# Performance work log

Hardware: AMD Instinct MI355X
Metric: run time of the kernel (lower is better)

Reference implementation:

```python
import jax, jax.numpy as jnp
import numpy as np

N_NODES = 40000
N_EDGES = 640000
IN_CH = 128
HID_CH = 128
OUT_CH = 121


def setup_inputs() -> dict:
    key = jax.random.key(0)
    ks = jax.random.split(key, 6)
    x = jax.random.normal(ks[0], (N_NODES, IN_CH), dtype=jnp.float32)
    edge_index = jax.random.randint(ks[1], (2, N_EDGES), 0, N_NODES, dtype=jnp.int64)

    def xavier(k, shape):
        fan_out, fan_in = shape
        lim = np.sqrt(6.0 / (fan_in + fan_out)).astype(np.float32)
        return jax.random.uniform(k, shape, jnp.float32, -lim, lim)

    W1l = xavier(ks[2], (HID_CH, IN_CH))
    W1r = xavier(ks[3], (HID_CH, IN_CH))
    W2l = xavier(ks[4], (OUT_CH, HID_CH))
    W2r = xavier(ks[5], (OUT_CH, HID_CH))
    b1l = jnp.zeros((HID_CH,), jnp.float32)
    b1r = jnp.zeros((HID_CH,), jnp.float32)
    b2l = jnp.zeros((OUT_CH,), jnp.float32)
    b2r = jnp.zeros((OUT_CH,), jnp.float32)
    return {"x": x, "edge_index": edge_index,
            "W1l": W1l, "b1l": b1l, "W1r": W1r, "b1r": b1r,
            "W2l": W2l, "b2l": b2l, "W2r": W2r, "b2r": b2r}


def _sage_conv(h, src, dst, Wl, bl, Wr, br):
    # mean aggregation of source-node features onto destinations
    msg = h[src]                                             # [E, C]
    agg = jax.ops.segment_sum(msg, dst, num_segments=N_NODES)
    cnt = jax.ops.segment_sum(jnp.ones((src.shape[0],), h.dtype), dst,
                              num_segments=N_NODES)
    agg = agg / jnp.maximum(cnt, 1.0)[:, None]
    # out = lin_l(agg) + lin_r(h)
    return agg @ Wl.T + bl + h @ Wr.T + br


def reference(x, edge_index, W1l, b1l, W1r, b1r, W2l, b2l, W2r, b2r):
    src, dst = edge_index[0], edge_index[1]
    h = jax.nn.relu(_sage_conv(x, src, dst, W1l, b1l, W1r, b1r))
    # dropout is identity in inference mode
    return _sage_conv(h, src, dst, W2l, b2l, W2r, b2r)
```

## Files before the change

kernel.cpp:

```cpp
#include <hip/hip_runtime.h>


#define NCH 128
#define CAPX 16
#define EPT 8

typedef __bf16 bf16x8 __attribute__((ext_vector_type(8)));
typedef float f32x4 __attribute__((ext_vector_type(4)));
typedef unsigned short ushort8 __attribute__((ext_vector_type(8)));

static __device__ __forceinline__ unsigned short f2b(float f) {
  return __builtin_bit_cast(unsigned short, static_cast<__bf16>(f));
}
static __device__ __forceinline__ float b2f(unsigned short u) {
  union { unsigned int i; float f; } v;
  v.i = ((unsigned int)u) << 16;
  return v.f;
}

__global__ __launch_bounds__(256) void k_main(
    const int* __restrict__ src, const int* __restrict__ dst, int E,
    int* __restrict__ cntx, unsigned short* __restrict__ slotu,
    int* __restrict__ ovf_n, int2* __restrict__ ovf,
    const float* __restrict__ x, unsigned short* __restrict__ xb, int n4,
    const float* __restrict__ W1l, const float* __restrict__ W1r,
    const float* __restrict__ b1l, const float* __restrict__ b1r,
    const float* __restrict__ W2l, const float* __restrict__ W2r,
    const float* __restrict__ b2l, const float* __restrict__ b2r,
    unsigned short* __restrict__ pack1, unsigned short* __restrict__ pack2,
    float* __restrict__ bsum1, float* __restrict__ bsum2, int NOUT,
    int nbBkt, int nbCvt) {
  int blk = blockIdx.x;
  if (blk < nbBkt) {
    unsigned int xcc;
    asm volatile("s_getreg_b32 %0, hwreg(HW_REG_XCC_ID)" : "=s"(xcc));
    xcc &= 7u;
    const int base = blk * (256 * EPT) + (int)threadIdx.x;
    int d[EPT], s[EPT], pos[EPT];
#pragma unroll
    for (int j = 0; j < EPT; ++j) {
      const int e = base + j * 256;
      const bool ok = e < E;
      d[j] = ok ? dst[e] : -1;
      s[j] = ok ? src[e] : 0;
    }
#pragma unroll
    for (int j = 0; j < EPT; ++j) {
      pos[j] = (d[j] >= 0)
          ? __hip_atomic_fetch_add(&cntx[(long)d[j] * 8 + xcc], 1,
                                   __ATOMIC_RELAXED, __HIP_MEMORY_SCOPE_WORKGROUP)
          : 0;
    }
#pragma unroll
    for (int j = 0; j < EPT; ++j) {
      if (d[j] >= 0) {
        if (pos[j] < CAPX)
          slotu[(long)d[j] * 128 + xcc * CAPX + pos[j]] = (unsigned short)s[j];
        else {
          int o = atomicAdd(ovf_n, 1);
          ovf[o] = make_int2(d[j], s[j]);
        }
      }
    }
    return;
  }
  blk -= nbBkt;
  if (blk < nbCvt) {
    int i = blk * 256 + threadIdx.x;
    if (i < n4) {
      float4 v = ((const float4*)x)[i];
      ushort4 r;
      r.x = f2b(v.x); r.y = f2b(v.y); r.z = f2b(v.z); r.w = f2b(v.w);
      ((ushort4*)xb)[i] = r;
    }
    return;
  }
  blk -= nbCvt;
  const int layer = blk >> 4;
  const float* Wl = layer ? W2l : W1l;
  const float* Wr = layer ? W2r : W1r;
  const float* bl = layer ? b2l : b1l;
  const float* br = layer ? b2r : b1r;
  unsigned short* pack = layer ? pack2 : pack1;
  float* bsum = layer ? bsum2 : bsum1;
  const int NO = layer ? NOUT : NCH;
  int tid = (blk & 15) * 256 + threadIdx.x;
  int c = tid >> 9;
  int t = (tid >> 6) & 7;
  int l = tid & 63;
  int n = t * 16 + (l & 15);
  int kb = c * 32 + ((l >> 4) << 3);
  unsigned short o[8];
#pragma unroll
  for (int j = 0; j < 8; ++j) {
    int k = kb + j;
    float v = 0.f;
    if (n < NO) v = (k < 128) ? Wl[n * 128 + k] : Wr[n * 128 + (k - 128)];
    o[j] = f2b(v);
  }
  ushort4 lo, hi;
  lo.x = o[0]; lo.y = o[1]; lo.z = o[2]; lo.w = o[3];
  hi.x = o[4]; hi.y = o[5]; hi.z = o[6]; hi.w = o[7];
  *(ushort4*)(pack + (long)tid * 8) = lo;
  *(ushort4*)(pack + (long)tid * 8 + 4) = hi;
  if (tid < 128) bsum[tid] = (tid < NO) ? (bl[tid] + br[tid]) : 0.f;
}

__global__ __launch_bounds__(256) void k_agg(
    const unsigned short* __restrict__ feat, const int* __restrict__ cntx,
    const unsigned short* __restrict__ slotu, const int* __restrict__ ovf_n,
    const int2* __restrict__ ovf, unsigned short* __restrict__ agg, int N) {
  __shared__ unsigned short list[16][128];
  __shared__ int degs[16], ms[16];
  const int lg = threadIdx.x >> 4;
  const int ln = threadIdx.x & 15;
  const int g = blockIdx.x * 16 + lg;

  if (g < N) {
    const int4 cA = *(const int4*)(cntx + (long)g * 8);
    const int4 cB = *(const int4*)(cntx + (long)g * 8 + 4);
    const int c[8] = {cA.x, cA.y, cA.z, cA.w, cB.x, cB.y, cB.z, cB.w};
    int deg = 0, p = 0, myoff = 0, mycc = 0;
#pragma unroll
    for (int xx = 0; xx < 8; ++xx) {
      const int cc = (c[xx] < CAPX) ? c[xx] : CAPX;
      if (ln == xx) { myoff = p; mycc = cc; }
      p += cc;
      deg += c[xx];
    }
    if (ln == 0) { degs[lg] = deg; ms[lg] = p; }
    if (ln < 8 && mycc > 0) {
      const unsigned short* sp = slotu + (long)g * 128 + ln * CAPX;
      for (int i = 0; i < mycc; ++i) list[lg][myoff + i] = sp[i];
    }
  } else if (ln == 0) {
    degs[lg] = 0; ms[lg] = 0;
  }
  __syncthreads();

  if (g >= N) return;
  const int m = ms[lg];
  const int col = ln * 8;
  const unsigned short* fcol = feat + col;

  float acc[8];
#pragma unroll
  for (int k = 0; k < 8; ++k) acc[k] = 0.f;

  const unsigned short* __restrict__ il = list[lg];
  int j = 0;
  for (; j + 7 < m; j += 8) {
    const int i0 = il[j + 0], i1 = il[j + 1], i2 = il[j + 2], i3 = il[j + 3];
    const int i4 = il[j + 4], i5 = il[j + 5], i6 = il[j + 6], i7 = il[j + 7];
    const ushort8 v0 = *(const ushort8*)(fcol + (long)i0 * NCH);
    const ushort8 v1 = *(const ushort8*)(fcol + (long)i1 * NCH);
    const ushort8 v2 = *(const ushort8*)(fcol + (long)i2 * NCH);
    const ushort8 v3 = *(const ushort8*)(fcol + (long)i3 * NCH);
    const ushort8 v4 = *(const ushort8*)(fcol + (long)i4 * NCH);
    const ushort8 v5 = *(const ushort8*)(fcol + (long)i5 * NCH);
    const ushort8 v6 = *(const ushort8*)(fcol + (long)i6 * NCH);
    const ushort8 v7 = *(const ushort8*)(fcol + (long)i7 * NCH);
#pragma unroll
    for (int k = 0; k < 8; ++k) {
      acc[k] += b2f(v0[k]); acc[k] += b2f(v1[k]);
      acc[k] += b2f(v2[k]); acc[k] += b2f(v3[k]);
      acc[k] += b2f(v4[k]); acc[k] += b2f(v5[k]);
      acc[k] += b2f(v6[k]); acc[k] += b2f(v7[k]);
    }
  }
  if (j + 3 < m) {
    const int i0 = il[j + 0], i1 = il[j + 1], i2 = il[j + 2], i3 = il[j + 3];
    const ushort8 v0 = *(const ushort8*)(fcol + (long)i0 * NCH);
    const ushort8 v1 = *(const ushort8*)(fcol + (long)i1 * NCH);
    const ushort8 v2 = *(const ushort8*)(fcol + (long)i2 * NCH);
    const ushort8 v3 = *(const ushort8*)(fcol + (long)i3 * NCH);
#pragma unroll
    for (int k = 0; k < 8; ++k) {
      acc[k] += b2f(v0[k]); acc[k] += b2f(v1[k]);
      acc[k] += b2f(v2[k]); acc[k] += b2f(v3[k]);
    }
    j += 4;
  }
  for (; j < m; ++j) {
    const ushort8 v = *(const ushort8*)(fcol + (long)il[j] * NCH);
#pragma unroll
    for (int k = 0; k < 8; ++k) acc[k] += b2f(v[k]);
  }

  const int on = *ovf_n;
  for (int o = 0; o < on; ++o) {
    const int2 p = ovf[o];
    if (p.x == g) {
      const ushort8 v = *(const ushort8*)(fcol + (long)p.y * NCH);
#pragma unroll
      for (int k = 0; k < 8; ++k) acc[k] += b2f(v[k]);
    }
  }

  const int deg = degs[lg];
  const int dd = (deg < 1) ? 1 : deg;
  const float inv = 1.f / (float)dd;
  ushort8 r;
#pragma unroll
  for (int k = 0; k < 8; ++k) r[k] = f2b(acc[k] * inv);
  *(ushort8*)(agg + (long)g * NCH + col) = r;
}

__global__ __launch_bounds__(256) void k_gemm(
    const unsigned short* __restrict__ Ag,
    const unsigned short* __restrict__ Sf,
    const unsigned short* __restrict__ pack,
    const float* __restrict__ bsum,
    unsigned short* __restrict__ outb,
    float* __restrict__ outf,
    int M, int NO, int do_relu) {
  const int wave = threadIdx.x >> 6;
  const int lane = threadIdx.x & 63;
  const int R = blockIdx.x * 128 + wave * 32;
  const int mrow = lane & 15;
  const int koct = (lane >> 4) * 8;

  int r0 = R + mrow;       if (r0 > M - 1) r0 = M - 1;
  int r1 = R + 16 + mrow;  if (r1 > M - 1) r1 = M - 1;

  f32x4 acc[2][8];
#pragma unroll
  for (int mt = 0; mt < 2; ++mt)
#pragma unroll
    for (int t = 0; t < 8; ++t) acc[mt][t] = (f32x4){0.f, 0.f, 0.f, 0.f};

#pragma unroll
  for (int c = 0; c < 8; ++c) {
    const unsigned short* __restrict__ Abase = (c < 4) ? Ag : Sf;
    const int k0 = (c & 3) * 32;
    const bf16x8 a0 = *(const bf16x8*)(Abase + (long)r0 * NCH + k0 + koct);
    const bf16x8 a1 = *(const bf16x8*)(Abase + (long)r1 * NCH + k0 + koct);
    const unsigned short* bp = pack + ((long)(c * 8) * 64 + lane) * 8;
#pragma unroll
    for (int t = 0; t < 8; ++t) {
      const bf16x8 bfrag = *(const bf16x8*)(bp + (long)t * 512);
      acc[0][t] = __builtin_amdgcn_mfma_f32_16x16x32_bf16(a0, bfrag, acc[0][t], 0, 0, 0);
      acc[1][t] = __builtin_amdgcn_mfma_f32_16x16x32_bf16(a1, bfrag, acc[1][t], 0, 0, 0);
    }
  }

  const int nloc = lane & 15;
  const int rquad = (lane >> 4) * 4;
#pragma unroll
  for (int mt = 0; mt < 2; ++mt) {
#pragma unroll
    for (int t = 0; t < 8; ++t) {
      const int n = t * 16 + nloc;
      const float bias = bsum[n];
#pragma unroll
      for (int r = 0; r < 4; ++r) {
        const int m = R + mt * 16 + rquad + r;
        if (m < M && n < NO) {
          float v = acc[mt][t][r] + bias;
          if (do_relu) v = fmaxf(v, 0.f);
          if (outb) outb[(long)m * NCH + n] = f2b(v);
          else outf[(long)m * NO + n] = v;
        }
      }
    }
  }
}


extern "C" void kernel_launch(void* const* d_in, const int* in_sizes, int n_in,
                              void* d_out, int out_size, void* d_ws, size_t ws_size,
                              hipStream_t stream) {
  const float* x = (const float*)d_in[0];
  const int* ei = (const int*)d_in[1];
  const float* W1l = (const float*)d_in[2];
  const float* b1l = (const float*)d_in[3];
  const float* W1r = (const float*)d_in[4];
  const float* b1r = (const float*)d_in[5];
  const float* W2l = (const float*)d_in[6];
  const float* b2l = (const float*)d_in[7];
  const float* W2r = (const float*)d_in[8];
  const float* b2r = (const float*)d_in[9];
  float* out = (float*)d_out;

  const int N = in_sizes[0] / NCH;
  const int E = in_sizes[1] / 2;
  const int NOUT = out_size / N;

  const int* src = ei;
  const int* dst = ei + E;

  char* w = (char*)d_ws;
  auto alloc = [&](size_t bytes) {
    char* p = w;
    w += (bytes + 255) & ~(size_t)255;
    return p;
  };
  unsigned short* xb = (unsigned short*)alloc((size_t)N * NCH * 2);
  unsigned short* hb = (unsigned short*)alloc((size_t)N * NCH * 2);
  unsigned short* aggb = (unsigned short*)alloc((size_t)N * NCH * 2);
  unsigned short* pack1 = (unsigned short*)alloc(8 * 8 * 64 * 8 * 2);
  unsigned short* pack2 = (unsigned short*)alloc(8 * 8 * 64 * 8 * 2);
  float* bsum1 = (float*)alloc(128 * 4);
  float* bsum2 = (float*)alloc(128 * 4);
  int* cntx = (int*)alloc(((size_t)N * 8 + 1) * 4);
  int* ovf_n = cntx + (size_t)N * 8;
  unsigned short* slotu = (unsigned short*)alloc((size_t)N * 128 * 2);
  int2* ovf = (int2*)alloc((size_t)E * 8);

  const int n4 = N * NCH / 4;
  const int nbBkt = (E + 256 * EPT - 1) / (256 * EPT);
  const int nbCvt = (n4 + 255) / 256;

  hipMemsetAsync(cntx, 0, ((size_t)N * 8 + 1) * 4, stream);

  k_main<<<nbBkt + nbCvt + 32, 256, 0, stream>>>(
      src, dst, E, cntx, slotu, ovf_n, ovf,
      x, xb, n4,
      W1l, W1r, b1l, b1r, W2l, W2r, b2l, b2r,
      pack1, pack2, bsum1, bsum2, NOUT, nbBkt, nbCvt);

  const int gaggr = (N + 15) / 16;
  const int gblk = (N + 127) / 128;

  k_agg<<<gaggr, 256, 0, stream>>>(xb, cntx, slotu, ovf_n, ovf, aggb, N);
  k_gemm<<<gblk, 256, 0, stream>>>(aggb, xb, pack1, bsum1, hb, (float*)nullptr,
                                   N, NCH, 1);
  k_agg<<<gaggr, 256, 0, stream>>>(hb, cntx, slotu, ovf_n, ovf, aggb, N);
  k_gemm<<<gblk, 256, 0, stream>>>(aggb, hb, pack2, bsum2, (unsigned short*)nullptr,
                                   out, N, NOUT, 0);
}
```

Measured before the change: 204.0 us.

## Fuse all stages into one persistent cooperative kernel with grid-wide syncs

Replaces the memset plus five kernel launches with a single cooperative persistent kernel that runs setup, bucketing, two aggregations and two GEMMs as grid-strided phases separated by grid.sync(). The memset of the count array moves into the setup phase. The aim is to remove launch gaps and the memset call. The grid is capped at 1024 blocks, so the gather-heavy aggregation may get less latency hiding than the original 2500-block launch, and each grid barrier adds its own cost. A fallback path launches the phases as separate kernels if the cooperative launch fails.

After: 213.4 us. 4.6% more time.

```diff
diff --git a/kernel.cpp b/kernel.cpp
--- a/kernel.cpp
+++ b/kernel.cpp
@@ -1,4 +1,7 @@
 #include <hip/hip_runtime.h>
+#include <hip/hip_cooperative_groups.h>
+
+namespace cg = cooperative_groups;
 
 
 #define NCH 128
@@ -18,36 +21,83 @@
   return v.f;
 }
 
-__global__ __launch_bounds__(256) void k_main(
-    const int* __restrict__ src, const int* __restrict__ dst, int E,
-    int* __restrict__ cntx, unsigned short* __restrict__ slotu,
-    int* __restrict__ ovf_n, int2* __restrict__ ovf,
-    const float* __restrict__ x, unsigned short* __restrict__ xb, int n4,
-    const float* __restrict__ W1l, const float* __restrict__ W1r,
-    const float* __restrict__ b1l, const float* __restrict__ b1r,
-    const float* __restrict__ W2l, const float* __restrict__ W2r,
-    const float* __restrict__ b2l, const float* __restrict__ b2r,
-    unsigned short* __restrict__ pack1, unsigned short* __restrict__ pack2,
-    float* __restrict__ bsum1, float* __restrict__ bsum2, int NOUT,
-    int nbBkt, int nbCvt) {
-  int blk = blockIdx.x;
-  if (blk < nbBkt) {
-    unsigned int xcc;
-    asm volatile("s_getreg_b32 %0, hwreg(HW_REG_XCC_ID)" : "=s"(xcc));
-    xcc &= 7u;
+struct Params {
+  const int* src; const int* dst; int E;
+  int* cntx; unsigned short* slotu; int* ovf_n; int2* ovf;
+  const float* x; unsigned short* xb; int n4;
+  const float* W1l; const float* W1r; const float* b1l; const float* b1r;
+  const float* W2l; const float* W2r; const float* b2l; const float* b2r;
+  unsigned short* pack1; unsigned short* pack2;
+  float* bsum1; float* bsum2;
+  unsigned short* aggb; unsigned short* hb;
+  float* out;
+  int N; int NOUT;
+};
+
+__device__ __forceinline__ void phase_setup(const Params& p) {
+  const int gthreads = gridDim.x * 256;
+  const int gtid = blockIdx.x * 256 + (int)threadIdx.x;
+  const int nz4 = p.N * 2;
+  const int4 z = {0, 0, 0, 0};
+  for (int i = gtid; i < nz4; i += gthreads) ((int4*)p.cntx)[i] = z;
+  if (gtid == 0) *p.ovf_n = 0;
+  for (int i = gtid; i < p.n4; i += gthreads) {
+    float4 v = ((const float4*)p.x)[i];
+    ushort4 r;
+    r.x = f2b(v.x); r.y = f2b(v.y); r.z = f2b(v.z); r.w = f2b(v.w);
+    ((ushort4*)p.xb)[i] = r;
+  }
+  for (int vt = gtid; vt < 8192; vt += gthreads) {
+    const int layer = vt >> 12;
+    const int tid2 = vt & 4095;
+    const float* Wl = layer ? p.W2l : p.W1l;
+    const float* Wr = layer ? p.W2r : p.W1r;
+    const float* bl = layer ? p.b2l : p.b1l;
+    const float* br = layer ? p.b2r : p.b1r;
+    unsigned short* pack = layer ? p.pack2 : p.pack1;
+    float* bsum = layer ? p.bsum2 : p.bsum1;
+    const int NO = layer ? p.NOUT : NCH;
+    const int c = tid2 >> 9;
+    const int t = (tid2 >> 6) & 7;
+    const int l = tid2 & 63;
+    const int n = t * 16 + (l & 15);
+    const int kb = c * 32 + ((l >> 4) << 3);
+    unsigned short o[8];
+#pragma unroll
+    for (int j = 0; j < 8; ++j) {
+      const int k = kb + j;
+      float v = 0.f;
+      if (n < NO) v = (k < 128) ? Wl[n * 128 + k] : Wr[n * 128 + (k - 128)];
+      o[j] = f2b(v);
+    }
+    ushort4 lo, hi;
+    lo.x = o[0]; lo.y = o[1]; lo.z = o[2]; lo.w = o[3];
+    hi.x = o[4]; hi.y = o[5]; hi.z = o[6]; hi.w = o[7];
+    *(ushort4*)(pack + (long)tid2 * 8) = lo;
+    *(ushort4*)(pack + (long)tid2 * 8 + 4) = hi;
+    if (tid2 < 128) bsum[tid2] = (tid2 < NO) ? (bl[tid2] + br[tid2]) : 0.f;
+  }
+}
+
+__device__ __forceinline__ void phase_bucket(const Params& p) {
+  unsigned int xcc;
+  asm volatile("s_getreg_b32 %0, hwreg(HW_REG_XCC_ID)" : "=s"(xcc));
+  xcc &= 7u;
+  const int nbBkt = (p.E + 256 * EPT - 1) / (256 * EPT);
+  for (int blk = blockIdx.x; blk < nbBkt; blk += gridDim.x) {
     const int base = blk * (256 * EPT) + (int)threadIdx.x;
     int d[EPT], s[EPT], pos[EPT];
 #pragma unroll
     for (int j = 0; j < EPT; ++j) {
       const int e = base + j * 256;
-      const bool ok = e < E;
-      d[j] = ok ? dst[e] : -1;
-      s[j] = ok ? src[e] : 0;
+      const bool ok = e < p.E;
+      d[j] = ok ? p.dst[e] : -1;
+      s[j] = ok ? p.src[e] : 0;
     }
 #pragma unroll
     for (int j = 0; j < EPT; ++j) {
       pos[j] = (d[j] >= 0)
-          ? __hip_atomic_fetch_add(&cntx[(long)d[j] * 8 + xcc], 1,
+          ? __hip_atomic_fetch_add(&p.cntx[(long)d[j] * 8 + xcc], 1,
                                    __ATOMIC_RELAXED, __HIP_MEMORY_SCOPE_WORKGROUP)
           : 0;
     }
@@ -55,239 +105,215 @@
     for (int j = 0; j < EPT; ++j) {
       if (d[j] >= 0) {
         if (pos[j] < CAPX)
-          slotu[(long)d[j] * 128 + xcc * CAPX + pos[j]] = (unsigned short)s[j];
+          p.slotu[(long)d[j] * 128 + xcc * CAPX + pos[j]] = (unsigned short)s[j];
         else {
-          int o = atomicAdd(ovf_n, 1);
-          ovf[o] = make_int2(d[j], s[j]);
-        }
-      }
-    }
-    return;
-  }
-  blk -= nbBkt;
-  if (blk < nbCvt) {
-    int i = blk * 256 + threadIdx.x;
-    if (i < n4) {
-      float4 v = ((const float4*)x)[i];
-      ushort4 r;
-      r.x = f2b(v.x); r.y = f2b(v.y); r.z = f2b(v.z); r.w = f2b(v.w);
-      ((ushort4*)xb)[i] = r;
-    }
-    return;
-  }
-  blk -= nbCvt;
-  const int layer = blk >> 4;
-  const float* Wl = layer ? W2l : W1l;
-  const float* Wr = layer ? W2r : W1r;
-  const float* bl = layer ? b2l : b1l;
-  const float* br = layer ? b2r : b1r;
-  unsigned short* pack = layer ? pack2 : pack1;
-  float* bsum = layer ? bsum2 : bsum1;
-  const int NO = layer ? NOUT : NCH;
-  int tid = (blk & 15) * 256 + threadIdx.x;
-  int c = tid >> 9;
-  int t = (tid >> 6) & 7;
-  int l = tid & 63;
-  int n = t * 16 + (l & 15);
-  int kb = c * 32 + ((l >> 4) << 3);
-  unsigned short o[8];
-#pragma unroll
-  for (int j = 0; j < 8; ++j) {
-    int k = kb + j;
-    float v = 0.f;
-    if (n < NO) v = (k < 128) ? Wl[n * 128 + k] : Wr[n * 128 + (k - 128)];
-    o[j] = f2b(v);
-  }
-  ushort4 lo, hi;
-  lo.x = o[0]; lo.y = o[1]; lo.z = o[2]; lo.w = o[3];
-  hi.x = o[4]; hi.y = o[5]; hi.z = o[6]; hi.w = o[7];
-  *(ushort4*)(pack + (long)tid * 8) = lo;
-  *(ushort4*)(pack + (long)tid * 8 + 4) = hi;
-  if (tid < 128) bsum[tid] = (tid < NO) ? (bl[tid] + br[tid]) : 0.f;
-}
-
-__global__ __launch_bounds__(256) void k_agg(
+          int o = atomicAdd(p.ovf_n, 1);
+          p.ovf[o] = make_int2(d[j], s[j]);
+        }
+      }
+    }
+  }
+}
+
+__device__ __forceinline__ void phase_agg(
     const unsigned short* __restrict__ feat, const int* __restrict__ cntx,
     const unsigned short* __restrict__ slotu, const int* __restrict__ ovf_n,
-    const int2* __restrict__ ovf, unsigned short* __restrict__ agg, int N) {
-  __shared__ unsigned short list[16][128];
-  __shared__ int degs[16], ms[16];
+    const int2* __restrict__ ovf, unsigned short* __restrict__ agg, int N,
+    unsigned short (*list)[128], int* degs, int* ms) {
   const int lg = threadIdx.x >> 4;
   const int ln = threadIdx.x & 15;
-  const int g = blockIdx.x * 16 + lg;
-
-  if (g < N) {
-    const int4 cA = *(const int4*)(cntx + (long)g * 8);
-    const int4 cB = *(const int4*)(cntx + (long)g * 8 + 4);
-    const int c[8] = {cA.x, cA.y, cA.z, cA.w, cB.x, cB.y, cB.z, cB.w};
-    int deg = 0, p = 0, myoff = 0, mycc = 0;
-#pragma unroll
-    for (int xx = 0; xx < 8; ++xx) {
-      const int cc = (c[xx] < CAPX) ? c[xx] : CAPX;
-      if (ln == xx) { myoff = p; mycc = cc; }
-      p += cc;
-      deg += c[xx];
-    }
-    if (ln == 0) { degs[lg] = deg; ms[lg] = p; }
-    if (ln < 8 && mycc > 0) {
-      const unsigned short* sp = slotu + (long)g * 128 + ln * CAPX;
-      for (int i = 0; i < mycc; ++i) list[lg][myoff + i] = sp[i];
-    }
-  } else if (ln == 0) {
-    degs[lg] = 0; ms[lg] = 0;
-  }
-  __syncthreads();
-
-  if (g >= N) return;
-  const int m = ms[lg];
-  const int col = ln * 8;
-  const unsigned short* fcol = feat + col;
-
-  float acc[8];
-#pragma unroll
-  for (int k = 0; k < 8; ++k) acc[k] = 0.f;
-
-  const unsigned short* __restrict__ il = list[lg];
-  int j = 0;
-  for (; j + 7 < m; j += 8) {
-    const int i0 = il[j + 0], i1 = il[j + 1], i2 = il[j + 2], i3 = il[j + 3];
-    const int i4 = il[j + 4], i5 = il[j + 5], i6 = il[j + 6], i7 = il[j + 7];
-    const ushort8 v0 = *(const ushort8*)(fcol + (long)i0 * NCH);
-    const ushort8 v1 = *(const ushort8*)(fcol + (long)i1 * NCH);
-    const ushort8 v2 = *(const ushort8*)(fcol + (long)i2 * NCH);
-    const ushort8 v3 = *(const ushort8*)(fcol + (long)i3 * NCH);
-    const ushort8 v4 = *(const ushort8*)(fcol + (long)i4 * NCH);
-    const ushort8 v5 = *(const ushort8*)(fcol + (long)i5 * NCH);
-    const ushort8 v6 = *(const ushort8*)(fcol + (long)i6 * NCH);
-    const ushort8 v7 = *(const ushort8*)(fcol + (long)i7 * NCH);
-#pragma unroll
-    for (int k = 0; k < 8; ++k) {
-      acc[k] += b2f(v0[k]); acc[k] += b2f(v1[k]);
-      acc[k] += b2f(v2[k]); acc[k] += b2f(v3[k]);
-      acc[k] += b2f(v4[k]); acc[k] += b2f(v5[k]);
-      acc[k] += b2f(v6[k]); acc[k] += b2f(v7[k]);
-    }
-  }
-  if (j + 3 < m) {
-    const int i0 = il[j + 0], i1 = il[j + 1], i2 = il[j + 2], i3 = il[j + 3];
-    const ushort8 v0 = *(const ushort8*)(fcol + (long)i0 * NCH);
-    const ushort8 v1 = *(const ushort8*)(fcol + (long)i1 * NCH);
-    const ushort8 v2 = *(const ushort8*)(fcol + (long)i2 * NCH);
-    const ushort8 v3 = *(const ushort8*)(fcol + (long)i3 * NCH);
-#pragma unroll
-    for (int k = 0; k < 8; ++k) {
-      acc[k] += b2f(v0[k]); acc[k] += b2f(v1[k]);
-      acc[k] += b2f(v2[k]); acc[k] += b2f(v3[k]);
-    }
-    j += 4;
-  }
-  for (; j < m; ++j) {
-    const ushort8 v = *(const ushort8*)(fcol + (long)il[j] * NCH);
-#pragma unroll
-    for (int k = 0; k < 8; ++k) acc[k] += b2f(v[k]);
-  }
-
-  const int on = *ovf_n;
-  for (int o = 0; o < on; ++o) {
-    const int2 p = ovf[o];
-    if (p.x == g) {
-      const ushort8 v = *(const ushort8*)(fcol + (long)p.y * NCH);
-#pragma unroll
-      for (int k = 0; k < 8; ++k) acc[k] += b2f(v[k]);
-    }
-  }
-
-  const int deg = degs[lg];
-  const int dd = (deg < 1) ? 1 : deg;
-  const float inv = 1.f / (float)dd;
-  ushort8 r;
-#pragma unroll
-  for (int k = 0; k < 8; ++k) r[k] = f2b(acc[k] * inv);
-  *(ushort8*)(agg + (long)g * NCH + col) = r;
-}
-
-__global__ __launch_bounds__(256) void k_gemm(
-    const unsigned short* __restrict__ Ag,
-    const unsigned short* __restrict__ Sf,
-    const unsigned short* __restrict__ pack,
-    const float* __restrict__ bsum,
-    unsigned short* __restrict__ outb,
-    float* __restrict__ outf,
+  const int nblk = (N + 15) / 16;
+  for (int gb = blockIdx.x; gb < nblk; gb += gridDim.x) {
+    const int g = gb * 16 + lg;
+    __syncthreads();
+    if (g < N) {
+      const int4 cA = *(const int4*)(cntx + (long)g * 8);
+      const int4 cB = *(const int4*)(cntx + (long)g * 8 + 4);
+      const int c[8] = {cA.x, cA.y, cA.z, cA.w, cB.x, cB.y, cB.z, cB.w};
+      int deg = 0, pp = 0, myoff = 0, mycc = 0;
+#pragma unroll
+      for (int xx = 0; xx < 8; ++xx) {
+        const int cc = (c[xx] < CAPX) ? c[xx] : CAPX;
+        if (ln == xx) { myoff = pp; mycc = cc; }
+        pp += cc;
+        deg += c[xx];
+      }
+      if (ln == 0) { degs[lg] = deg; ms[lg] = pp; }
+      if (ln < 8 && mycc > 0) {
+        const unsigned short* sp = slotu + (long)g * 128 + ln * CAPX;
+        for (int i = 0; i < mycc; ++i) list[lg][myoff + i] = sp[i];
+      }
+    } else if (ln == 0) {
+      degs[lg] = 0; ms[lg] = 0;
+    }
+    __syncthreads();
+
+    if (g < N) {
+      const int m = ms[lg];
+      const int col = ln * 8;
+      const unsigned short* fcol = feat + col;
+      float acc[8];
+#pragma unroll
+      for (int k = 0; k < 8; ++k) acc[k] = 0.f;
+      const unsigned short* __restrict__ il = list[lg];
+      int j = 0;
+      for (; j + 7 < m; j += 8) {
+        const int i0 = il[j + 0], i1 = il[j + 1], i2 = il[j + 2], i3 = il[j + 3];
+        const int i4 = il[j + 4], i5 = il[j + 5], i6 = il[j + 6], i7 = il[j + 7];
+        const ushort8 v0 = *(const ushort8*)(fcol + (long)i0 * NCH);
+        const ushort8 v1 = *(const ushort8*)(fcol + (long)i1 * NCH);
+        const ushort8 v2 = *(const ushort8*)(fcol + (long)i2 * NCH);
+        const ushort8 v3 = *(const ushort8*)(fcol + (long)i3 * NCH);
+        const ushort8 v4 = *(const ushort8*)(fcol + (long)i4 * NCH);
+        const ushort8 v5 = *(const ushort8*)(fcol + (long)i5 * NCH);
+        const ushort8 v6 = *(const ushort8*)(fcol + (long)i6 * NCH);
+        const ushort8 v7 = *(const ushort8*)(fcol + (long)i7 * NCH);
+#pragma unroll
+        for (int k = 0; k < 8; ++k) {
+          acc[k] += b2f(v0[k]); acc[k] += b2f(v1[k]);
+          acc[k] += b2f(v2[k]); acc[k] += b2f(v3[k]);
+          acc[k] += b2f(v4[k]); acc[k] += b2f(v5[k]);
+          acc[k] += b2f(v6[k]); acc[k] += b2f(v7[k]);
+        }
+      }
+      if (j + 3 < m) {
+        const int i0 = il[j + 0], i1 = il[j + 1], i2 = il[j + 2], i3 = il[j + 3];
+        const ushort8 v0 = *(const ushort8*)(fcol + (long)i0 * NCH);
+        const ushort8 v1 = *(const ushort8*)(fcol + (long)i1 * NCH);
+        const ushort8 v2 = *(const ushort8*)(fcol + (long)i2 * NCH);
+        const ushort8 v3 = *(const ushort8*)(fcol + (long)i3 * NCH);
+#pragma unroll
+        for (int k = 0; k < 8; ++k) {
+          acc[k] += b2f(v0[k]); acc[k] += b2f(v1[k]);
+          acc[k] += b2f(v2[k]); acc[k] += b2f(v3[k]);
+        }
+        j += 4;
+      }
+      for (; j < m; ++j) {
+        const ushort8 v = *(const ushort8*)(fcol + (long)il[j] * NCH);
+#pragma unroll
+        for (int k = 0; k < 8; ++k) acc[k] += b2f(v[k]);
+      }
+      const int on = *ovf_n;
+      for (int o = 0; o < on; ++o) {
+        const int2 pr = ovf[o];
+        if (pr.x == g) {
+          const ushort8 v = *(const ushort8*)(fcol + (long)pr.y * NCH);
+#pragma unroll
+          for (int k = 0; k < 8; ++k) acc[k] += b2f(v[k]);
+        }
+      }
+      const int deg = degs[lg];
+      const int dd = (deg < 1) ? 1 : deg;
+      const float inv = 1.f / (float)dd;
+      ushort8 r;
+#pragma unroll
+      for (int k = 0; k < 8; ++k) r[k] = f2b(acc[k] * inv);
+      *(ushort8*)(agg + (long)g * NCH + col) = r;
+    }
+  }
+}
+
+__device__ __forceinline__ void phase_gemm(
+    const unsigned short* __restrict__ Ag, const unsigned short* __restrict__ Sf,
+    const unsigned short* __restrict__ pack, const float* __restrict__ bsum,
+    unsigned short* __restrict__ outb, float* __restrict__ outf,
     int M, int NO, int do_relu) {
   const int wave = threadIdx.x >> 6;
   const int lane = threadIdx.x & 63;
-  const int R = blockIdx.x * 128 + wave * 32;
   const int mrow = lane & 15;
   const int koct = (lane >> 4) * 8;
-
-  int r0 = R + mrow;       if (r0 > M - 1) r0 = M - 1;
-  int r1 = R + 16 + mrow;  if (r1 > M - 1) r1 = M - 1;
-
-  f32x4 acc[2][8];
-#pragma unroll
-  for (int mt = 0; mt < 2; ++mt)
-#pragma unroll
-    for (int t = 0; t < 8; ++t) acc[mt][t] = (f32x4){0.f, 0.f, 0.f, 0.f};
-
-#pragma unroll
-  for (int c = 0; c < 8; ++c) {
-    const unsigned short* __restrict__ Abase = (c < 4) ? Ag : Sf;
-    const int k0 = (c & 3) * 32;
-    const bf16x8 a0 = *(const bf16x8*)(Abase + (long)r0 * NCH + k0 + koct);
-    const bf16x8 a1 = *(const bf16x8*)(Abase + (long)r1 * NCH + k0 + koct);
-    const unsigned short* bp = pack + ((long)(c * 8) * 64 + lane) * 8;
-#pragma unroll
-    for (int t = 0; t < 8; ++t) {
-      const bf16x8 bfrag = *(const bf16x8*)(bp + (long)t * 512);
-      acc[0][t] = __builtin_amdgcn_mfma_f32_16x16x32_bf16(a0, bfrag, acc[0][t], 0, 0, 0);
-      acc[1][t] = __builtin_amdgcn_mfma_f32_16x16x32_bf16(a1, bfrag, acc[1][t], 0, 0, 0);
-    }
-  }
-
   const int nloc = lane & 15;
   const int rquad = (lane >> 4) * 4;
-#pragma unroll
-  for (int mt = 0; mt < 2; ++mt) {
-#pragma unroll
-    for (int t = 0; t < 8; ++t) {
-      const int n = t * 16 + nloc;
-      const float bias = bsum[n];
-#pragma unroll
-      for (int r = 0; r < 4; ++r) {
-        const int m = R + mt * 16 + rquad + r;
-        if (m < M && n < NO) {
-          float v = acc[mt][t][r] + bias;
-          if (do_relu) v = fmaxf(v, 0.f);
-          if (outb) outb[(long)m * NCH + n] = f2b(v);
-          else outf[(long)m * NO + n] = v;
-        }
-      }
-    }
-  }
+  const int ntile = (M + 127) / 128;
+
+  for (int tile = blockIdx.x; tile < ntile; tile += gridDim.x) {
+    const int R = tile * 128 + wave * 32;
+    int r0 = R + mrow;       if (r0 > M - 1) r0 = M - 1;
+    int r1 = R + 16 + mrow;  if (r1 > M - 1) r1 = M - 1;
+
+    f32x4 acc[2][8];
+#pragma unroll
+    for (int mt = 0; mt < 2; ++mt)
+#pragma unroll
+      for (int t = 0; t < 8; ++t) acc[mt][t] = (f32x4){0.f, 0.f, 0.f, 0.f};
+
+#pragma unroll
+    for (int c = 0; c < 8; ++c) {
+      const unsigned short* __restrict__ Abase = (c < 4) ? Ag : Sf;
+      const int k0 = (c & 3) * 32;
+      const bf16x8 a0 = *(const bf16x8*)(Abase + (long)r0 * NCH + k0 + koct);
+      const bf16x8 a1 = *(const bf16x8*)(Abase + (long)r1 * NCH + k0 + koct);
+      const unsigned short* bp = pack + ((long)(c * 8) * 64 + lane) * 8;
+#pragma unroll
+      for (int t = 0; t < 8; ++t) {
+        const bf16x8 bfrag = *(const bf16x8*)(bp + (long)t * 512);
+        acc[0][t] = __builtin_amdgcn_mfma_f32_16x16x32_bf16(a0, bfrag, acc[0][t], 0, 0, 0);
+        acc[1][t] = __builtin_amdgcn_mfma_f32_16x16x32_bf16(a1, bfrag, acc[1][t], 0, 0, 0);
+      }
+    }
+
+#pragma unroll
+    for (int mt = 0; mt < 2; ++mt) {
+#pragma unroll
+      for (int t = 0; t < 8; ++t) {
+        const int n = t * 16 + nloc;
+        const float bias = bsum[n];
+#pragma unroll
+        for (int r = 0; r < 4; ++r) {
+          const int m = R + mt * 16 + rquad + r;
+          if (m < M && n < NO) {
+            float v = acc[mt][t][r] + bias;
+            if (do_relu) v = fmaxf(v, 0.f);
+            if (outb) outb[(long)m * NCH + n] = f2b(v);
+            else outf[(long)m * NO + n] = v;
+          }
+        }
+      }
+    }
+  }
+}
+
+__global__ __launch_bounds__(256) void k_all(Params p) {
+  cg::grid_group grid = cg::this_grid();
+  __shared__ unsigned short list[16][128];
+  __shared__ int degs[16], ms[16];
+
+  phase_setup(p);
+  grid.sync();
+  phase_bucket(p);
+  grid.sync();
+  phase_agg(p.xb, p.cntx, p.slotu, p.ovf_n, p.ovf, p.aggb, p.N, list, degs, ms);
+  grid.sync();
+  phase_gemm(p.aggb, p.xb, p.pack1, p.bsum1, p.hb, (float*)nullptr, p.N, NCH, 1);
+  grid.sync();
+  phase_agg(p.hb, p.cntx, p.slotu, p.ovf_n, p.ovf, p.aggb, p.N, list, degs, ms);
+  grid.sync();
+  phase_gemm(p.aggb, p.hb, p.pack2, p.bsum2, (unsigned short*)nullptr, p.out,
+             p.N, p.NOUT, 0);
+}
+
+__global__ __launch_bounds__(256) void k_p_setup(Params p) { phase_setup(p); }
+__global__ __launch_bounds__(256) void k_p_bucket(Params p) { phase_bucket(p); }
+__global__ __launch_bounds__(256) void k_p_agg(Params p, const unsigned short* feat) {
+  __shared__ unsigned short list[16][128];
+  __shared__ int degs[16], ms[16];
+  phase_agg(feat, p.cntx, p.slotu, p.ovf_n, p.ovf, p.aggb, p.N, list, degs, ms);
+}
+__global__ __launch_bounds__(256) void k_p_gemm(
+    const unsigned short* Ag, const unsigned short* Sf,
+    const unsigned short* pack, const float* bsum,
+    unsigned short* outb, float* outf, int M, int NO, int do_relu) {
+  phase_gemm(Ag, Sf, pack, bsum, outb, outf, M, NO, do_relu);
 }
 
 
 extern "C" void kernel_launch(void* const* d_in, const int* in_sizes, int n_in,
                               void* d_out, int out_size, void* d_ws, size_t ws_size,
                               hipStream_t stream) {
-  const float* x = (const float*)d_in[0];
-  const int* ei = (const int*)d_in[1];
-  const float* W1l = (const float*)d_in[2];
-  const float* b1l = (const float*)d_in[3];
-  const float* W1r = (const float*)d_in[4];
-  const float* b1r = (const float*)d_in[5];
-  const float* W2l = (const float*)d_in[6];
-  const float* b2l = (const float*)d_in[7];
-  const float* W2r = (const float*)d_in[8];
-  const float* b2r = (const float*)d_in[9];
-  float* out = (float*)d_out;
-
   const int N = in_sizes[0] / NCH;
   const int E = in_sizes[1] / 2;
   const int NOUT = out_size / N;
-
-  const int* src = ei;
-  const int* dst = ei + E;
 
   char* w = (char*)d_ws;
   auto alloc = [&](size_t bytes) {
@@ -302,30 +328,55 @@
   unsigned short* pack2 = (unsigned short*)alloc(8 * 8 * 64 * 8 * 2);
   float* bsum1 = (float*)alloc(128 * 4);
   float* bsum2 = (float*)alloc(128 * 4);
-  int* cntx = (int*)alloc(((size_t)N * 8 + 1) * 4);
+  int* cntx = (int*)alloc(((size_t)N * 8 + 4) * 4);
   int* ovf_n = cntx + (size_t)N * 8;
   unsigned short* slotu = (unsigned short*)alloc((size_t)N * 128 * 2);
   int2* ovf = (int2*)alloc((size_t)E * 8);
 
-  const int n4 = N * NCH / 4;
-  const int nbBkt = (E + 256 * EPT - 1) / (256 * EPT);
-  const int nbCvt = (n4 + 255) / 256;
-
-  hipMemsetAsync(cntx, 0, ((size_t)N * 8 + 1) * 4, stream);
-
-  k_main<<<nbBkt + nbCvt + 32, 256, 0, stream>>>(
-      src, dst, E, cntx, slotu, ovf_n, ovf,
-      x, xb, n4,
-      W1l, W1r, b1l, b1r, W2l, W2r, b2l, b2r,
-      pack1, pack2, bsum1, bsum2, NOUT, nbBkt, nbCvt);
-
-  const int gaggr = (N + 15) / 16;
-  const int gblk = (N + 127) / 128;
-
-  k_agg<<<gaggr, 256, 0, stream>>>(xb, cntx, slotu, ovf_n, ovf, aggb, N);
-  k_gemm<<<gblk, 256, 0, stream>>>(aggb, xb, pack1, bsum1, hb, (float*)nullptr,
-                                   N, NCH, 1);
-  k_agg<<<gaggr, 256, 0, stream>>>(hb, cntx, slotu, ovf_n, ovf, aggb, N);
-  k_gemm<<<gblk, 256, 0, stream>>>(aggb, hb, pack2, bsum2, (unsigned short*)nullptr,
-                                   out, N, NOUT, 0);
-}
+  Params p;
+  p.src = (const int*)d_in[1];
+  p.dst = ((const int*)d_in[1]) + E;
+  p.E = E;
+  p.cntx = cntx; p.slotu = slotu; p.ovf_n = ovf_n; p.ovf = ovf;
+  p.x = (const float*)d_in[0]; p.xb = xb; p.n4 = N * NCH / 4;
+  p.W1l = (const float*)d_in[2]; p.b1l = (const float*)d_in[3];
+  p.W1r = (const float*)d_in[4]; p.b1r = (const float*)d_in[5];
+  p.W2l = (const float*)d_in[6]; p.b2l = (const float*)d_in[7];
+  p.W2r = (const float*)d_in[8]; p.b2r = (const float*)d_in[9];
+  p.pack1 = pack1; p.pack2 = pack2; p.bsum1 = bsum1; p.bsum2 = bsum2;
+  p.aggb = aggb; p.hb = hb;
+  p.out = (float*)d_out;
+  p.N = N; p.NOUT = NOUT;
+
+  int dev = 0;
+  hipGetDevice(&dev);
+  int ncu = 0;
+  hipDeviceGetAttribute(&ncu, hipDeviceAttributeMultiprocessorCount, dev);
+  int occ = 0;
+  hipOccupancyMaxActiveBlocksPerMultiprocessor(&occ, k_all, 256, 0);
+
+  bool launched = false;
+  if (occ > 0 && ncu > 0) {
+    int grid = occ * ncu;
+    if (grid > 1024) grid = 1024;
+    void* args[] = {&p};
+    hipError_t err = hipLaunchCooperativeKernel((const void*)k_all, dim3(grid),
+                                                dim3(256), args, 0, stream);
+    launched = (err == hipSuccess);
+  }
+
+  if (!launched) {
+    const int gagg = (N + 15) / 16;
+    const int gtile = (N + 127) / 128;
+    const int gbkt = (E + 256 * EPT - 1) / (256 * EPT);
+    k_p_setup<<<1024, 256, 0, stream>>>(p);
+    k_p_bucket<<<gbkt, 256, 0, stream>>>(p);
+    k_p_agg<<<gagg, 256, 0, stream>>>(p, xb);
+    k_p_gemm<<<gtile, 256, 0, stream>>>(aggb, xb, pack1, bsum1, hb,
+                                        (float*)nullptr, N, NCH, 1);
+    k_p_agg<<<gagg, 256, 0, stream>>>(p, hb);
+    k_p_gemm<<<gtile, 256, 0, stream>>>(aggb, hb, pack2, bsum2,
+                                        (unsigned short*)nullptr, (float*)d_out,
+                                        N, NOUT, 0);
+  }
+}
```
